# Performance work log

Measured on AMD Instinct MI355X. Metric: run time of the kernel, lower is better.

## Reference

```python
import jax, jax.numpy as jnp
import numpy as np

N, C, EMB, OUT, HID, HEADS, K, R, E = 100000, 256, 256, 8, 256, 4, 20000, 16, 800000
RETR_IN = EMB + OUT + 1  # z_retr + o_retr + retr_score
DH = HID // HEADS


def _lin(key, fi, fo):
    return jax.random.normal(key, (fi, fo), jnp.float32) / np.sqrt(fi)


def setup_inputs() -> dict:
    key = jax.random.key(0)
    ks = jax.random.split(key, 32)
    inp = {
        "h_cone": jax.random.normal(ks[0], (N, C), jnp.float32),
        "z_retr": jax.random.normal(ks[1], (K, R, EMB), jnp.float32),
        "o_retr": jax.random.normal(ks[2], (K, R, OUT), jnp.float32),
        "retr_score": jax.random.uniform(ks[3], (K, R), jnp.float32),
        "teacher_yhat": jax.random.normal(ks[4], (N, OUT), jnp.float32),
        "outpin_nids": jax.random.randint(ks[5], (K,), 0, N, jnp.int32),
        "edge_index": jax.random.randint(ks[6], (2, E), 0, N, jnp.int32),
        # retr_proj: Linear(RETR_IN,HID) -> ReLU -> Linear(HID,HID)
        "rp_W1": _lin(ks[7], RETR_IN, HID), "rp_b1": jnp.zeros((HID,), jnp.float32),
        "rp_W2": _lin(ks[8], HID, HID),     "rp_b2": jnp.zeros((HID,), jnp.float32),
        # query_proj: Linear(C, HID)
        "qp_W": _lin(ks[9], C, HID), "qp_b": jnp.zeros((HID,), jnp.float32),
        # MultiheadAttention packed q/k/v projection + output projection
        "in_proj_W": _lin(ks[10], HID, 3 * HID), "in_proj_b": jnp.zeros((3 * HID,), jnp.float32),
        "out_proj_W": _lin(ks[11], HID, HID),    "out_proj_b": jnp.zeros((HID,), jnp.float32),
        # gate_net: Linear(C+HID,HID) -> ReLU -> Linear(HID,C) -> Sigmoid
        "gate_W1": _lin(ks[12], C + HID, HID), "gate_b1": jnp.zeros((HID,), jnp.float32),
        "gate_W2": _lin(ks[13], HID, C),       "gate_b2": jnp.zeros((C,), jnp.float32),
        # update_net: Linear(HID,C) -> ReLU -> Linear(C,C)
        "upd_W1": _lin(ks[14], HID, C), "upd_b1": jnp.zeros((C,), jnp.float32),
        "upd_W2": _lin(ks[15], C, C),   "upd_b2": jnp.zeros((C,), jnp.float32),
        # cone GNN (LocalGNN gcn, 2 layers): C->HID, HID->HID with sym-normalized aggregation
        "gnn_W1": _lin(ks[16], C, HID),   "gnn_b1": jnp.zeros((HID,), jnp.float32),
        "gnn_W2": _lin(ks[17], HID, HID), "gnn_b2": jnp.zeros((HID,), jnp.float32),
        # head: Linear(HID,HID) -> ReLU -> Linear(HID,OUT) (orig zero-init; random here for nontrivial grads)
        "head_W1": _lin(ks[18], HID, HID), "head_b1": jnp.zeros((HID,), jnp.float32),
        "head_W2": _lin(ks[19], HID, OUT) * 0.01, "head_b2": jnp.zeros((OUT,), jnp.float32),
    }
    return inp


def _forward(h_cone, z_retr, o_retr, retr_score, teacher_yhat, outpin_nids, edge_index,
             rp_W1, rp_b1, rp_W2, rp_b2, qp_W, qp_b, in_proj_W, in_proj_b,
             out_proj_W, out_proj_b, gate_W1, gate_b1, gate_W2, gate_b2,
             upd_W1, upd_b1, upd_W2, upd_b2, gnn_W1, gnn_b1, gnn_W2, gnn_b2,
             head_W1, head_b1, head_W2, head_b2):
    # ---- retrieval aggregation: per-outpin cross-attn over R neighbors ----
    kv_in = jnp.concatenate([z_retr, o_retr, retr_score[..., None]], axis=-1)  # [K,R,RETR_IN]
    kv = jax.nn.relu(kv_in @ rp_W1 + rp_b1) @ rp_W2 + rp_b2                    # [K,R,HID]
    hq = h_cone[outpin_nids]                                                   # [K,C] gather
    q = hq @ qp_W + qp_b                                                       # [K,HID]
    Wq, Wk, Wv = jnp.split(in_proj_W, 3, axis=1)
    bq, bk, bv = jnp.split(in_proj_b, 3)
    qh = (q @ Wq + bq).reshape(K, HEADS, DH)
    kh = (kv @ Wk + bk).reshape(K, R, HEADS, DH)
    vh = (kv @ Wv + bv).reshape(K, R, HEADS, DH)
    att = jax.nn.softmax(jnp.einsum('khd,krhd->khr', qh, kh) / np.sqrt(DH), axis=-1)
    ctx = jnp.einsum('khr,krhd->khd', att, vh).reshape(K, HID)
    retr_ctx = ctx @ out_proj_W + out_proj_b                                   # [K,HID]
    # ---- gated outpin fusion + scatter back ----
    gate = jax.nn.sigmoid(jax.nn.relu(jnp.concatenate([hq, retr_ctx], axis=-1) @ gate_W1 + gate_b1) @ gate_W2 + gate_b2)
    update = jax.nn.relu(retr_ctx @ upd_W1 + upd_b1) @ upd_W2 + upd_b2         # [K,C]
    h = h_cone.at[outpin_nids].set(hq + gate * update)                         # scatter
    # ---- cone GNN: 2-layer GCN with self loops, symmetric normalization ----
    loops = jnp.arange(N, dtype=edge_index.dtype)
    src = jnp.concatenate([edge_index[0], loops])
    dst = jnp.concatenate([edge_index[1], loops])
    deg = jax.ops.segment_sum(jnp.ones_like(src, jnp.float32), dst, num_segments=N)
    norm = (jax.lax.rsqrt(deg[src]) * jax.lax.rsqrt(deg[dst]))[:, None]
    x1 = h @ gnn_W1 + gnn_b1
    h1 = jax.nn.relu(jax.ops.segment_sum(x1[src] * norm, dst, num_segments=N))
    x2 = h1 @ gnn_W2 + gnn_b2
    h2 = jax.ops.segment_sum(x2[src] * norm, dst, num_segments=N)
    # ---- residual head ----
    delta = jax.nn.relu(h2 @ head_W1 + head_b1) @ head_W2 + head_b2
    return teacher_yhat + delta


def reference(h_cone, z_retr, o_retr, retr_score, teacher_yhat, outpin_nids, edge_index,
              rp_W1, rp_b1, rp_W2, rp_b2, qp_W, qp_b, in_proj_W, in_proj_b,
              out_proj_W, out_proj_b, gate_W1, gate_b1, gate_W2, gate_b2,
              upd_W1, upd_b1, upd_W2, upd_b2, gnn_W1, gnn_b1, gnn_W2, gnn_b2,
              head_W1, head_b1, head_W2, head_b2):
    return _forward(h_cone, z_retr, o_retr, retr_score, teacher_yhat, outpin_nids, edge_index,
                    rp_W1, rp_b1, rp_W2, rp_b2, qp_W, qp_b, in_proj_W, in_proj_b,
                    out_proj_W, out_proj_b, gate_W1, gate_b1, gate_W2, gate_b2,
                    upd_W1, upd_b1, upd_W2, upd_b2, gnn_W1, gnn_b1, gnn_W2, gnn_b2,
                    head_W1, head_b1, head_W2, head_b2)
```

## Files before the change

kernel.cpp:

```cpp
#include <hip/hip_runtime.h>
#include <cstdint>
#include <cstddef>

typedef unsigned short u16;

#define NN    100000
#define OUTD  8
#define KKP   20000
#define RR    16
#define EE    800000
#define KRR   (KKP*RR)
#define KP    20096
#define NP    100096

typedef __bf16 v8bf __attribute__((ext_vector_type(8)));
typedef float  v4f  __attribute__((ext_vector_type(4)));

__device__ __forceinline__ float b2f(u16 u) {
    union { uint32_t i; float f; } v; v.i = (uint32_t)u << 16; return v.f;
}
__device__ __forceinline__ u16 f2b(float f) {
    union { float f; uint32_t i; } v; v.f = f;
    uint32_t i = v.i;
    return (u16)((i + 0x7fffu + ((i >> 16) & 1u)) >> 16);
}
__device__ __forceinline__ uint32_t pk2(float a, float b) {
    return (uint32_t)f2b(a) | ((uint32_t)f2b(b) << 16);
}

#define GLDS(g, l) __builtin_amdgcn_global_load_lds(                         \
    (const __attribute__((address_space(1))) void*)(g),                      \
    (__attribute__((address_space(3))) void*)(l), 16, 0, 0)

template <int EPI, int OMODE, int A32, int RETR>
__launch_bounds__(256)
__global__ void gemm_bf_k(const void* __restrict__ Av, int lda, int M, int Ka,
                          const u16* __restrict__ Wt,
                          const float* __restrict__ bias,
                          void* __restrict__ Cv, int ldc,
                          const float* __restrict__ o_ex,
                          const float* __restrict__ s_ex,
                          const float* __restrict__ Wex)
{
    __shared__ u16 As[128 * 32];
    __shared__ u16 Bs[128 * 32];
    const int row0 = blockIdx.x * 128;
    const int col0 = blockIdx.y * 128;
    const int t    = threadIdx.x;
    const int lane = t & 63;
    const int w    = t >> 6;
    const int wm   = w & 1, wn = w >> 1;

    const int idx0 = t, idx1 = t + 256;
    const u16* Ab = (const u16*)Av;
    const float* Af = (const float*)Av;
    const u16* Ag0 = Ab + (size_t)(row0 + (idx0 >> 2)) * lda + (idx0 & 3) * 8;
    const u16* Ag1 = Ab + (size_t)(row0 + (idx1 >> 2)) * lda + (idx1 & 3) * 8;
    const float* Af0 = Af + (size_t)(row0 + (idx0 >> 2)) * lda + (idx0 & 3) * 8;
    const float* Af1 = Af + (size_t)(row0 + (idx1 >> 2)) * lda + (idx1 & 3) * 8;
    const u16* Bg0 = Wt + (size_t)(col0 + (idx0 >> 2)) * Ka + (idx0 & 3) * 8;
    const u16* Bg1 = Wt + (size_t)(col0 + (idx1 >> 2)) * Ka + (idx1 & 3) * 8;
    u16* Asp0 = &As[idx0 * 8];
    u16* Asp1 = &As[idx1 * 8];
    u16* Bsp0 = &Bs[idx0 * 8];
    u16* Bsp1 = &Bs[idx1 * 8];

    v4f acc[4][4];
#pragma unroll
    for (int mi = 0; mi < 4; mi++)
#pragma unroll
        for (int ni = 0; ni < 4; ni++) acc[mi][ni] = 0.f;

    const int fr = lane & 15;
    const int fq = (lane >> 4) * 8;

    for (int kk = 0; kk < Ka; kk += 32) {
        float4 a00, a01, a10, a11;
        if (A32) {
            a00 = *(const float4*)(Af0 + kk);
            a01 = *(const float4*)(Af0 + kk + 4);
            a10 = *(const float4*)(Af1 + kk);
            a11 = *(const float4*)(Af1 + kk + 4);
        }
        __syncthreads();
        if (A32) {
            uint4 u0, u1;
            u0.x = pk2(a00.x, a00.y); u0.y = pk2(a00.z, a00.w);
            u0.z = pk2(a01.x, a01.y); u0.w = pk2(a01.z, a01.w);
            u1.x = pk2(a10.x, a10.y); u1.y = pk2(a10.z, a10.w);
            u1.z = pk2(a11.x, a11.y); u1.w = pk2(a11.z, a11.w);
            *(uint4*)Asp0 = u0;
            *(uint4*)Asp1 = u1;
        } else {
            GLDS(Ag0 + kk, Asp0);
            GLDS(Ag1 + kk, Asp1);
        }
        GLDS(Bg0 + kk, Bsp0);
        GLDS(Bg1 + kk, Bsp1);
        __syncthreads();
        v8bf af[4], bv[4];
#pragma unroll
        for (int mi = 0; mi < 4; mi++)
            af[mi] = *(const v8bf*)&As[(wm * 64 + mi * 16 + fr) * 32 + fq];
#pragma unroll
        for (int ni = 0; ni < 4; ni++)
            bv[ni] = *(const v8bf*)&Bs[(wn * 64 + ni * 16 + fr) * 32 + fq];
#pragma unroll
        for (int mi = 0; mi < 4; mi++)
#pragma unroll
            for (int ni = 0; ni < 4; ni++)
                acc[mi][ni] = __builtin_amdgcn_mfma_f32_16x16x32_bf16(
                    af[mi], bv[ni], acc[mi][ni], 0, 0, 0);
    }

    const int crow = wm * 64 + (lane >> 4) * 4;
    const int ccol = wn * 64 + (lane & 15);
    float bias_v[4];
#pragma unroll
    for (int ni = 0; ni < 4; ni++) bias_v[ni] = bias[col0 + ccol + ni * 16];

    u16*   Cb = (u16*)Cv;
    float* Cf = (float*)Cv;
#pragma unroll
    for (int mi = 0; mi < 4; mi++) {
#pragma unroll
        for (int reg = 0; reg < 4; reg++) {
            int r = row0 + crow + mi * 16 + reg;
            if (r >= M) continue;
            float ov[8], sv;
            if (RETR) {
#pragma unroll
                for (int u = 0; u < 8; u++) ov[u] = o_ex[(size_t)r * 8 + u];
                sv = s_ex[r];
            }
#pragma unroll
            for (int ni = 0; ni < 4; ni++) {
                int c = col0 + ccol + ni * 16;
                float v = acc[mi][ni][reg] + bias_v[ni];
                if (RETR) {
                    float e = sv * Wex[8 * 256 + c];
#pragma unroll
                    for (int u = 0; u < 8; u++) e = fmaf(ov[u], Wex[u * 256 + c], e);
                    v += e;
                }
                if (EPI == 1) v = fmaxf(v, 0.f);
                if (EPI == 2) v = 1.f / (1.f + expf(-v));
                if (OMODE == 1) Cb[(size_t)r * ldc + c] = f2b(v);
                else            Cf[(size_t)r * ldc + c] = v;
            }
        }
    }
}

__global__ void wtpose_k(const float* __restrict__ W, int ld, int coloff,
                         int fi, int Kpad, u16* __restrict__ Wt)
{
    int g = blockIdx.x * 256 + threadIdx.x;
    if (g >= 256 * Kpad) return;
    int o = g / Kpad, i = g - o * Kpad;
    Wt[g] = f2b(i < fi ? W[(size_t)i * ld + coloff + o] : 0.f);
}

__global__ void wfuse_k(const float* __restrict__ A, const float* __restrict__ Binw,
                        int ldb, int off, const float* __restrict__ ba,
                        const float* __restrict__ bb,
                        u16* __restrict__ Wt_out, float* __restrict__ bias_out)
{
    __shared__ float As[256];
    __shared__ float bs[256];
    int i = blockIdx.x, j = threadIdx.x;
    As[j] = A[(size_t)i * 256 + j];
    bs[j] = ba[j];
    __syncthreads();
    float acc = 0.f, accb = 0.f;
    for (int m = 0; m < 256; m++) {
        float bv = Binw[(size_t)m * ldb + off + j];
        acc = fmaf(As[m], bv, acc);
        if (i == 0) accb = fmaf(bs[m], bv, accb);
    }
    Wt_out[(size_t)j * 256 + i] = f2b(acc);
    if (i == 0) bias_out[j] = bb[j] + accb;
}

__global__ void conv_f2b_k(const float* __restrict__ src, u16* __restrict__ dst, size_t n4)
{
    size_t g = (size_t)blockIdx.x * 256 + threadIdx.x;
    if (g >= n4) return;
    float4 v = ((const float4*)src)[g];
    ((ushort4*)dst)[g] = make_ushort4(f2b(v.x), f2b(v.y), f2b(v.z), f2b(v.w));
}

__global__ void gather_hq_k(const float* __restrict__ hc, const int* __restrict__ nids,
                            u16* __restrict__ acat)
{
    int t = threadIdx.x;
    int k = blockIdx.x * 4 + (t >> 6);
    int c = t & 63;
    if (k >= KKP) return;
    int nid = nids[k];
    float4 v = ((const float4*)hc)[(size_t)nid * 64 + c];
    *(ushort4*)&acat[(size_t)k * 512 + c * 4] =
        make_ushort4(f2b(v.x), f2b(v.y), f2b(v.z), f2b(v.w));
}

__launch_bounds__(256)
__global__ void att_fused_k(const u16* __restrict__ qh, const u16* __restrict__ khv,
                            u16* __restrict__ ctx)
{
    int k = blockIdx.x;
    int t = threadIdx.x;
    int lane = t & 63;
    float qv = b2f(qh[(size_t)k * 256 + t]);
    const u16* kp = khv + (size_t)k * (RR * 512) + t;
    const u16* vp = kp + 256;
    float myscore = -1e30f;
#pragma unroll
    for (int r = 0; r < RR; r++) {
        float p = qv * b2f(kp[r * 512]);
#pragma unroll
        for (int off = 1; off < 64; off <<= 1) p += __shfl_xor(p, off);
        if (lane == r) myscore = p * 0.125f;
    }
    float m = (lane < RR) ? myscore : -1e30f;
#pragma unroll
    for (int off = 1; off < 16; off <<= 1) m = fmaxf(m, __shfl_xor(m, off));
    float pe = (lane < RR) ? expf(myscore - m) : 0.f;
    float ssum = pe;
#pragma unroll
    for (int off = 1; off < 16; off <<= 1) ssum += __shfl_xor(ssum, off);
    float pn = pe / ssum;
    float acc = 0.f;
#pragma unroll
    for (int r = 0; r < RR; r++) {
        float ar = __shfl(pn, r);
        acc = fmaf(ar, b2f(vp[r * 512]), acc);
    }
    ctx[(size_t)k * 256 + t] = f2b(acc);
}

__global__ void winner_k(const int* __restrict__ nids, int* __restrict__ winner)
{
    int gid = blockIdx.x * 256 + threadIdx.x;
    if (gid < KKP) atomicMax(&winner[nids[gid]], gid);
}

__global__ void scatter_h_k(const int* __restrict__ nids, const int* __restrict__ winner,
                            const float* __restrict__ hc, const float* __restrict__ gate,
                            const float* __restrict__ upd, u16* __restrict__ hb)
{
    int t = threadIdx.x;
    int k = blockIdx.x * 4 + (t >> 6);
    int c = t & 63;
    if (k >= KKP) return;
    int nid = nids[k];
    if (winner[nid] != k) return;
    float4 hv = ((const float4*)hc)[(size_t)nid * 64 + c];
    float4 gv = ((const float4*)gate)[(size_t)k * 64 + c];
    float4 uv = ((const float4*)upd)[(size_t)k * 64 + c];
    *(ushort4*)&hb[(size_t)nid * 256 + c * 4] = make_ushort4(
        f2b(hv.x + gv.x * uv.x), f2b(hv.y + gv.y * uv.y),
        f2b(hv.z + gv.z * uv.z), f2b(hv.w + gv.w * uv.w));
}

__global__ void edge_count_k(const int* __restrict__ dst, int* __restrict__ cnt, int e)
{
    int gid = blockIdx.x * 256 + threadIdx.x;
    if (gid < e) atomicAdd(&cnt[dst[gid]], 1);
}

__global__ void isd_k(const int* __restrict__ cnt, float* __restrict__ isd, int n)
{
    int gid = blockIdx.x * 256 + threadIdx.x;
    if (gid < n) isd[gid] = rsqrtf((float)(cnt[gid] + 1));
}

#define SCANB 1024
__global__ void scan1_k(const int* __restrict__ in, int* __restrict__ out,
                        int* __restrict__ bsums, int n)
{
    __shared__ int s[SCANB];
    int tid = threadIdx.x;
    int gid = blockIdx.x * SCANB + tid;
    int v = (gid < n) ? in[gid] : 0;
    s[tid] = v;
    __syncthreads();
    for (int off = 1; off < SCANB; off <<= 1) {
        int add = (tid >= off) ? s[tid - off] : 0;
        __syncthreads();
        s[tid] += add;
        __syncthreads();
    }
    if (gid < n) out[gid] = s[tid] - v;
    if (tid == SCANB - 1) bsums[blockIdx.x] = s[tid];
}

__global__ void scan2_k(int* bsums, int nb)
{
    if (threadIdx.x == 0 && blockIdx.x == 0) {
        int run = 0;
        for (int i = 0; i < nb; i++) { int v = bsums[i]; bsums[i] = run; run += v; }
    }
}

__global__ void scan3_k(int* __restrict__ out, const int* __restrict__ bsums, int n, int total)
{
    int gid = blockIdx.x * SCANB + threadIdx.x;
    if (gid < n) out[gid] += bsums[blockIdx.x];
    if (gid == 0) out[n] = total;
}

__global__ void csr_scatter_k(const int* __restrict__ src, const int* __restrict__ dst,
                              const int* __restrict__ row_start, int* __restrict__ cursor,
                              const float* __restrict__ isd,
                              int* __restrict__ csr_src, float* __restrict__ csr_w, int e)
{
    int gid = blockIdx.x * 256 + threadIdx.x;
    if (gid < e) {
        int sP = src[gid], dP = dst[gid];
        int pos = row_start[dP] + atomicAdd(&cursor[dP], 1);
        csr_src[pos] = sP;
        csr_w[pos] = isd[sP] * isd[dP];
    }
}

template <int RELU>
__launch_bounds__(256)
__global__ void gnn_agg_k(const u16* __restrict__ x, const int* __restrict__ row_start,
                          const int* __restrict__ csr_src, const float* __restrict__ csr_w,
                          const float* __restrict__ isd, u16* __restrict__ outp)
{
    int node = blockIdx.x * 4 + (threadIdx.x >> 6);
    int lane = threadIdx.x & 63;
    if (node >= NN) return;
    float si = isd[node];
    float sii = si * si;
    ushort4 sv = ((const ushort4*)x)[(size_t)node * 64 + lane];
    float a0 = b2f(sv.x) * sii, a1 = b2f(sv.y) * sii;
    float a2 = b2f(sv.z) * sii, a3 = b2f(sv.w) * sii;
    int s0 = row_start[node], s1 = row_start[node + 1];
    for (int j = s0; j < s1; j++) {
        int sP = csr_src[j];
        float wv = csr_w[j];
        ushort4 v = ((const ushort4*)x)[(size_t)sP * 64 + lane];
        a0 = fmaf(b2f(v.x), wv, a0);
        a1 = fmaf(b2f(v.y), wv, a1);
        a2 = fmaf(b2f(v.z), wv, a2);
        a3 = fmaf(b2f(v.w), wv, a3);
    }
    if (RELU) {
        a0 = fmaxf(a0, 0.f); a1 = fmaxf(a1, 0.f);
        a2 = fmaxf(a2, 0.f); a3 = fmaxf(a3, 0.f);
    }
    ((ushort4*)outp)[(size_t)node * 64 + lane] =
        make_ushort4(f2b(a0), f2b(a1), f2b(a2), f2b(a3));
}

__launch_bounds__(256)
__global__ void head_out_k(const u16* __restrict__ thid, const float* __restrict__ W2,
                           const float* __restrict__ b2, const float* __restrict__ teacher,
                           float* __restrict__ outp, int n)
{
    __shared__ float ts[32][257];
    __shared__ float w2s[256 * 8];
    int t = threadIdx.x;
    int rbase = blockIdx.x * 32;
    for (int i = t; i < 2048; i += 256) w2s[i] = W2[i];
    for (int i = t; i < 32 * 256; i += 256) {
        int rr = i >> 8, cc = i & 255;
        int gr = rbase + rr;
        ts[rr][cc] = (gr < n) ? b2f(thid[(size_t)gr * 256 + cc]) : 0.f;
    }
    __syncthreads();
    int rr = t >> 3, cc = t & 7;
    int gr = rbase + rr;
    if (gr >= n) return;
    float acc = b2[cc];
    for (int kk = 0; kk < 256; kk++)
        acc = fmaf(ts[rr][kk], w2s[kk * 8 + cc], acc);
    outp[(size_t)gr * 8 + cc] = teacher[(size_t)gr * 8 + cc] + acc;
}

extern "C" void kernel_launch(void* const* d_in, const int* in_sizes, int n_in,
                              void* d_out, int out_size, void* d_ws, size_t ws_size,
                              hipStream_t stream)
{
    (void)in_sizes; (void)n_in; (void)out_size; (void)ws_size;
    const float* h_cone     = (const float*)d_in[0];
    const float* z_retr     = (const float*)d_in[1];
    const float* o_retr     = (const float*)d_in[2];
    const float* retr_score = (const float*)d_in[3];
    const float* teacher    = (const float*)d_in[4];
    const int*   nids       = (const int*)d_in[5];
    const int*   edge       = (const int*)d_in[6];
    const float* rp_W1 = (const float*)d_in[7];   const float* rp_b1 = (const float*)d_in[8];
    const float* rp_W2 = (const float*)d_in[9];   const float* rp_b2 = (const float*)d_in[10];
    const float* qp_W  = (const float*)d_in[11];  const float* qp_b  = (const float*)d_in[12];
    const float* inW   = (const float*)d_in[13];  const float* inB   = (const float*)d_in[14];
    const float* outW  = (const float*)d_in[15];  const float* outB  = (const float*)d_in[16];
    const float* gW1   = (const float*)d_in[17];  const float* gB1   = (const float*)d_in[18];
    const float* gW2   = (const float*)d_in[19];  const float* gB2   = (const float*)d_in[20];
    const float* uW1   = (const float*)d_in[21];  const float* uB1   = (const float*)d_in[22];
    const float* uW2   = (const float*)d_in[23];  const float* uB2   = (const float*)d_in[24];
    const float* gnW1  = (const float*)d_in[25];  const float* gnB1  = (const float*)d_in[26];
    const float* gnW2  = (const float*)d_in[27];  const float* gnB2  = (const float*)d_in[28];
    const float* hW1   = (const float*)d_in[29];  const float* hB1   = (const float*)d_in[30];
    const float* hW2   = (const float*)d_in[31];  const float* hB2   = (const float*)d_in[32];
    float* out = (float*)d_out;

    char* ws = (char*)d_ws;
    size_t off = 0;
    auto alloc = [&](size_t bytes) -> void* {
        void* p = ws + off;
        off = (off + bytes + 255) & ~(size_t)255;
        return p;
    };
    u16* hidden = (u16*)alloc((size_t)KRR * 256 * 2);
    u16* khv    = (u16*)alloc((size_t)KRR * 512 * 2);
    u16* qhb    = (u16*)alloc((size_t)KP * 256 * 2);
    u16* ctxb   = (u16*)alloc((size_t)KP * 256 * 2);
    u16* acat   = (u16*)alloc((size_t)KP * 512 * 2);
    u16* ghid   = (u16*)alloc((size_t)KP * 256 * 2);
    float* gate = (float*)alloc((size_t)KP * 256 * 4);
    u16* uhid   = (u16*)alloc((size_t)KP * 256 * 2);
    float* upd  = (float*)alloc((size_t)KP * 256 * 4);
    u16* wt_rp1 = (u16*)alloc(256 * 256 * 2);
    u16* wt_kv  = (u16*)alloc(512 * 256 * 2);
    u16* wt_qf  = (u16*)alloc(256 * 256 * 2);
    u16* wt_o   = (u16*)alloc(256 * 256 * 2);
    u16* wt_g1  = (u16*)alloc(256 * 512 * 2);
    u16* wt_g2  = (u16*)alloc(256 * 256 * 2);
    u16* wt_u1  = (u16*)alloc(256 * 256 * 2);
    u16* wt_u2  = (u16*)alloc(256 * 256 * 2);
    u16* wt_gn1 = (u16*)alloc(256 * 256 * 2);
    u16* wt_gn2 = (u16*)alloc(256 * 256 * 2);
    u16* wt_h1  = (u16*)alloc(256 * 256 * 2);
    float* bias_kv = (float*)alloc(512 * 4);
    float* bias_qf = (float*)alloc(256 * 4);
    int*   winner    = (int*)alloc(NN * 4);
    int*   cnt       = (int*)alloc(NN * 4);
    int*   cursor    = (int*)alloc(NN * 4);
    int*   row_start = (int*)alloc((NN + 1) * 4);
    int*   bsums     = (int*)alloc(1024 * 4);
    float* isd       = (float*)alloc(NN * 4);
    int*   csr_src   = (int*)alloc((size_t)EE * 4);
    float* csr_w     = (float*)alloc((size_t)EE * 4);

    const size_t NPE = (size_t)NP * 256;
    u16* gZ0 = hidden;
    u16* gZ1 = hidden + NPE;
    u16* gZ2 = hidden + 2 * NPE;

    const int* esrc = edge;
    const int* edst = edge + EE;

    auto wtp = [&](const float* W, int ld, int coloff, int fi, int Kpad, u16* Wt) {
        wtpose_k<<<(256 * Kpad + 255) / 256, 256, 0, stream>>>(W, ld, coloff, fi, Kpad, Wt);
    };

    hipMemsetAsync(cnt, 0, NN * 4, stream);
    hipMemsetAsync(cursor, 0, NN * 4, stream);
    edge_count_k<<<(EE + 255) / 256, 256, 0, stream>>>(edst, cnt, EE);
    isd_k<<<(NN + 255) / 256, 256, 0, stream>>>(cnt, isd, NN);
    int nb = (NN + SCANB - 1) / SCANB;
    scan1_k<<<nb, SCANB, 0, stream>>>(cnt, row_start, bsums, NN);
    scan2_k<<<1, 64, 0, stream>>>(bsums, nb);
    scan3_k<<<nb, SCANB, 0, stream>>>(row_start, bsums, NN, EE);
    csr_scatter_k<<<(EE + 255) / 256, 256, 0, stream>>>(esrc, edst, row_start, cursor, isd,
                                                        csr_src, csr_w, EE);

    wtp(rp_W1, 256, 0, 256, 256, wt_rp1);
    wfuse_k<<<256, 256, 0, stream>>>(rp_W2, inW, 768, 256, rp_b2, inB + 256, wt_kv, bias_kv);
    wfuse_k<<<256, 256, 0, stream>>>(rp_W2, inW, 768, 512, rp_b2, inB + 512,
                                     wt_kv + 256 * 256, bias_kv + 256);
    wfuse_k<<<256, 256, 0, stream>>>(qp_W, inW, 768, 0, qp_b, inB, wt_qf, bias_qf);
    wtp(outW, 256, 0, 256, 256, wt_o);
    wtp(gW1,  256, 0, 512, 512, wt_g1);
    wtp(gW2,  256, 0, 256, 256, wt_g2);
    wtp(uW1,  256, 0, 256, 256, wt_u1);
    wtp(uW2,  256, 0, 256, 256, wt_u2);
    wtp(gnW1, 256, 0, 256, 256, wt_gn1);
    wtp(gnW2, 256, 0, 256, 256, wt_gn2);
    wtp(hW1,  256, 0, 256, 256, wt_h1);
    gather_hq_k<<<(KKP + 3) / 4, 256, 0, stream>>>(h_cone, nids, acat);

    gemm_bf_k<1, 1, 1, 1><<<dim3(KRR / 128, 2), 256, 0, stream>>>(
        z_retr, 256, KRR, 256, wt_rp1, rp_b1, hidden, 256,
        o_retr, retr_score, rp_W1 + 256 * 256);
    gemm_bf_k<0, 1, 0, 0><<<dim3(KRR / 128, 4), 256, 0, stream>>>(
        hidden, 256, KRR, 256, wt_kv, bias_kv, khv, 512, nullptr, nullptr, nullptr);
    gemm_bf_k<0, 1, 0, 0><<<dim3((KKP + 127) / 128, 2), 256, 0, stream>>>(
        acat, 512, KKP, 256, wt_qf, bias_qf, qhb, 256, nullptr, nullptr, nullptr);

    att_fused_k<<<KKP, 256, 0, stream>>>(qhb, khv, ctxb);
    gemm_bf_k<0, 1, 0, 0><<<dim3((KKP + 127) / 128, 2), 256, 0, stream>>>(
        ctxb, 256, KKP, 256, wt_o, outB, acat + 256, 512, nullptr, nullptr, nullptr);

    gemm_bf_k<1, 1, 0, 0><<<dim3((KKP + 127) / 128, 2), 256, 0, stream>>>(
        acat, 512, KKP, 512, wt_g1, gB1, ghid, 256, nullptr, nullptr, nullptr);
    gemm_bf_k<2, 2, 0, 0><<<dim3((KKP + 127) / 128, 2), 256, 0, stream>>>(
        ghid, 256, KKP, 256, wt_g2, gB2, gate, 256, nullptr, nullptr, nullptr);
    gemm_bf_k<1, 1, 0, 0><<<dim3((KKP + 127) / 128, 2), 256, 0, stream>>>(
        acat + 256, 512, KKP, 256, wt_u1, uB1, uhid, 256, nullptr, nullptr, nullptr);
    gemm_bf_k<0, 2, 0, 0><<<dim3((KKP + 127) / 128, 2), 256, 0, stream>>>(
        uhid, 256, KKP, 256, wt_u2, uB2, upd, 256, nullptr, nullptr, nullptr);

    conv_f2b_k<<<(int)(((size_t)NN * 64 + 255) / 256), 256, 0, stream>>>(
        h_cone, gZ0, (size_t)NN * 64);
    hipMemsetAsync(winner, 0xFF, NN * 4, stream);
    winner_k<<<(KKP + 255) / 256, 256, 0, stream>>>(nids, winner);
    scatter_h_k<<<(KKP + 3) / 4, 256, 0, stream>>>(nids, winner, h_cone, gate, upd, gZ0);

    gemm_bf_k<0, 1, 0, 0><<<dim3((NN + 127) / 128, 2), 256, 0, stream>>>(
        gZ0, 256, NN, 256, wt_gn1, gnB1, gZ1, 256, nullptr, nullptr, nullptr);
    gnn_agg_k<1><<<(NN + 3) / 4, 256, 0, stream>>>(gZ1, row_start, csr_src, csr_w, isd, gZ2);
    gemm_bf_k<0, 1, 0, 0><<<dim3((NN + 127) / 128, 2), 256, 0, stream>>>(
        gZ2, 256, NN, 256, wt_gn2, gnB2, gZ0, 256, nullptr, nullptr, nullptr);
    gnn_agg_k<0><<<(NN + 3) / 4, 256, 0, stream>>>(gZ0, row_start, csr_src, csr_w, isd, gZ1);
    gemm_bf_k<1, 1, 0, 0><<<dim3((NN + 127) / 128, 2), 256, 0, stream>>>(
        gZ1, 256, NN, 256, wt_h1, hB1, gZ2, 256, nullptr, nullptr, nullptr);
    head_out_k<<<(NN + 31) / 32, 256, 0, stream>>>(gZ2, hW2, hB2, teacher, out, NN);
}
```

Baseline: 1.794 ms.

## Triple-buffer GEMM LDS tiles with software-pipelined async global loads

Restructures the bf16 MFMA GEMM main loop into a multi-stage pipeline. B, and A when it is already bf16, go into three LDS buffers loaded two iterations ahead, while fp32 A is prefetched into registers and written to double-buffered LDS after the MFMAs. Explicit vmcnt waits and a single barrier per iteration replace the two __syncthreads per K step. The goal is to hide global-memory latency behind MFMA work, at the cost of more LDS, which may lower occupancy, and fragile hand-counted waitcnt values.

```diff
diff --git a/kernel.cpp b/kernel.cpp
--- a/kernel.cpp
+++ b/kernel.cpp
@@ -31,6 +31,9 @@
 #define GLDS(g, l) __builtin_amdgcn_global_load_lds(                         \
     (const __attribute__((address_space(1))) void*)(g),                      \
     (__attribute__((address_space(3))) void*)(l), 16, 0, 0)
+
+#define WAITVL(n) asm volatile("s_waitcnt vmcnt(" #n ") lgkmcnt(0)" ::: "memory")
+#define BAR() __builtin_amdgcn_s_barrier()
 
 template <int EPI, int OMODE, int A32, int RETR>
 __launch_bounds__(256)
@@ -42,8 +45,9 @@
                           const float* __restrict__ s_ex,
                           const float* __restrict__ Wex)
 {
-    __shared__ u16 As[128 * 32];
-    __shared__ u16 Bs[128 * 32];
+    constexpr int NBA = A32 ? 2 : 3;
+    __shared__ u16 As[NBA * 128 * 32];
+    __shared__ u16 Bs[3 * 128 * 32];
     const int row0 = blockIdx.x * 128;
     const int col0 = blockIdx.y * 128;
     const int t    = threadIdx.x;
@@ -60,10 +64,48 @@
     const float* Af1 = Af + (size_t)(row0 + (idx1 >> 2)) * lda + (idx1 & 3) * 8;
     const u16* Bg0 = Wt + (size_t)(col0 + (idx0 >> 2)) * Ka + (idx0 & 3) * 8;
     const u16* Bg1 = Wt + (size_t)(col0 + (idx1 >> 2)) * Ka + (idx1 & 3) * 8;
-    u16* Asp0 = &As[idx0 * 8];
-    u16* Asp1 = &As[idx1 * 8];
-    u16* Bsp0 = &Bs[idx0 * 8];
-    u16* Bsp1 = &Bs[idx1 * 8];
+    const int s0 = idx0 * 8, s1 = idx1 * 8;
+
+    auto stageB = [&](int bi, int kk) {
+        u16* bp = Bs + bi * (128 * 32);
+        GLDS(Bg0 + kk, bp + s0);
+        GLDS(Bg1 + kk, bp + s1);
+    };
+    auto stageA = [&](int bi, int kk) {
+        u16* ap = As + bi * (128 * 32);
+        GLDS(Ag0 + kk, ap + s0);
+        GLDS(Ag1 + kk, ap + s1);
+    };
+
+    float4 P0, P1, P2, P3, Q0, Q1, Q2, Q3;
+    auto loadP = [&](int kk) {
+        P0 = *(const float4*)(Af0 + kk);     P1 = *(const float4*)(Af0 + kk + 4);
+        P2 = *(const float4*)(Af1 + kk);     P3 = *(const float4*)(Af1 + kk + 4);
+    };
+    auto loadQ = [&](int kk) {
+        Q0 = *(const float4*)(Af0 + kk);     Q1 = *(const float4*)(Af0 + kk + 4);
+        Q2 = *(const float4*)(Af1 + kk);     Q3 = *(const float4*)(Af1 + kk + 4);
+    };
+    auto writeP = [&](int bi) {
+        u16* ap = As + bi * (128 * 32);
+        uint4 u0, u1;
+        u0.x = pk2(P0.x, P0.y); u0.y = pk2(P0.z, P0.w);
+        u0.z = pk2(P1.x, P1.y); u0.w = pk2(P1.z, P1.w);
+        u1.x = pk2(P2.x, P2.y); u1.y = pk2(P2.z, P2.w);
+        u1.z = pk2(P3.x, P3.y); u1.w = pk2(P3.z, P3.w);
+        *(uint4*)(ap + s0) = u0;
+        *(uint4*)(ap + s1) = u1;
+    };
+    auto writeQ = [&](int bi) {
+        u16* ap = As + bi * (128 * 32);
+        uint4 u0, u1;
+        u0.x = pk2(Q0.x, Q0.y); u0.y = pk2(Q0.z, Q0.w);
+        u0.z = pk2(Q1.x, Q1.y); u0.w = pk2(Q1.z, Q1.w);
+        u1.x = pk2(Q2.x, Q2.y); u1.y = pk2(Q2.z, Q2.w);
+        u1.z = pk2(Q3.x, Q3.y); u1.w = pk2(Q3.z, Q3.w);
+        *(uint4*)(ap + s0) = u0;
+        *(uint4*)(ap + s1) = u1;
+    };
 
     v4f acc[4][4];
 #pragma unroll
@@ -73,44 +115,64 @@
 
     const int fr = lane & 15;
     const int fq = (lane >> 4) * 8;
-
-    for (int kk = 0; kk < Ka; kk += 32) {
-        float4 a00, a01, a10, a11;
-        if (A32) {
-            a00 = *(const float4*)(Af0 + kk);
-            a01 = *(const float4*)(Af0 + kk + 4);
-            a10 = *(const float4*)(Af1 + kk);
-            a11 = *(const float4*)(Af1 + kk + 4);
+    const int nk = Ka >> 5;
+
+    if (A32) {
+        loadP(0);
+        stageB(0, 0);
+        if (nk > 1) {
+            loadQ(32);
+            stageB(1, 32);
         }
-        __syncthreads();
-        if (A32) {
-            uint4 u0, u1;
-            u0.x = pk2(a00.x, a00.y); u0.y = pk2(a00.z, a00.w);
-            u0.z = pk2(a01.x, a01.y); u0.w = pk2(a01.z, a01.w);
-            u1.x = pk2(a10.x, a10.y); u1.y = pk2(a10.z, a10.w);
-            u1.z = pk2(a11.x, a11.y); u1.w = pk2(a11.z, a11.w);
-            *(uint4*)Asp0 = u0;
-            *(uint4*)Asp1 = u1;
-        } else {
-            GLDS(Ag0 + kk, Asp0);
-            GLDS(Ag1 + kk, Asp1);
+        writeP(0);
+        if (nk > 1) { WAITVL(6); }
+        else        { WAITVL(0); }
+    } else {
+        stageA(0, 0); stageB(0, 0);
+        if (nk > 1) { stageA(1, 32); stageB(1, 32); WAITVL(4); }
+        else        { WAITVL(0); }
+    }
+    BAR();
+
+    int rb = 0, sb = 2;
+    for (int tI = 0; tI < nk; ++tI) {
+        const bool st = (tI + 2) < nk;
+        const int kk2 = (tI + 2) << 5;
+        if (st) {
+            if (A32) {
+                if (tI & 1) loadQ(kk2); else loadP(kk2);
+                stageB(sb, kk2);
+            } else {
+                stageA(sb, kk2);
+                stageB(sb, kk2);
+            }
         }
-        GLDS(Bg0 + kk, Bsp0);
-        GLDS(Bg1 + kk, Bsp1);
-        __syncthreads();
+        const u16* Ar = As + (A32 ? (tI & 1) : rb) * (128 * 32);
+        const u16* Br = Bs + rb * (128 * 32);
         v8bf af[4], bv[4];
 #pragma unroll
         for (int mi = 0; mi < 4; mi++)
-            af[mi] = *(const v8bf*)&As[(wm * 64 + mi * 16 + fr) * 32 + fq];
+            af[mi] = *(const v8bf*)&Ar[(wm * 64 + mi * 16 + fr) * 32 + fq];
 #pragma unroll
         for (int ni = 0; ni < 4; ni++)
-            bv[ni] = *(const v8bf*)&Bs[(wn * 64 + ni * 16 + fr) * 32 + fq];
+            bv[ni] = *(const v8bf*)&Br[(wn * 64 + ni * 16 + fr) * 32 + fq];
 #pragma unroll
         for (int mi = 0; mi < 4; mi++)
 #pragma unroll
             for (int ni = 0; ni < 4; ni++)
                 acc[mi][ni] = __builtin_amdgcn_mfma_f32_16x16x32_bf16(
                     af[mi], bv[ni], acc[mi][ni], 0, 0, 0);
+
+        if (tI + 1 < nk) {
+            if (A32) {
+                if (tI & 1) writeP((tI + 1) & 1); else writeQ((tI + 1) & 1);
+            }
+            if (st) { if (A32) { WAITVL(6); } else { WAITVL(4); } }
+            else    { WAITVL(0); }
+            BAR();
+        }
+        rb = (rb == 2) ? 0 : rb + 1;
+        sb = (sb == 2) ? 0 : sb + 1;
     }
 
     const int crow = wm * 64 + (lane >> 4) * 4;
```

Result: no change. 1.812 ms (+1.0%).
